# Performance work log

Measured on AMD Instinct MI355X. Metric: run time of the kernel, lower is better.

## Reference

```python
import jax, jax.numpy as jnp
import numpy as np


def _segmented_exclusive_cumsum(vals, seg_start_flags):
    """Exclusive cumsum of vals that resets at segment starts (flags True)."""
    def combine(a, b):
        va, fa = a
        vb, fb = b
        return (jnp.where(fb, vb, va + vb), fa | fb)
    inclusive, _ = jax.lax.associative_scan(combine, (vals, seg_start_flags))
    return inclusive - vals


def setup_inputs() -> dict:
    key = jax.random.key(0)
    k1, k2 = jax.random.split(key)
    n_rays = 65536
    samples_per_ray = 128  # average; ragged via sorted random ray ids
    n_pts = n_rays * samples_per_ray  # 8_388_608 sample points
    density = jax.random.normal(k1, (n_pts,), dtype=jnp.float32)
    ray_id = jnp.sort(jax.random.randint(k2, (n_pts,), 0, n_rays)).astype(jnp.int32)
    shift = jnp.float32(-3.0)      # self.act_shift
    interval = jnp.float32(0.5)    # stepsize * voxel_size_ratio
    return {"density": density, "shift": shift, "interval": interval,
            "ray_id": ray_id, "n_rays": n_rays}


def reference(density, shift, interval, ray_id, n_rays):
    # Raw2Alpha: alpha = 1 - exp(-softplus(density + shift) * interval)
    # log(1 - alpha) = -interval * softplus(density + shift)  (stable, no log of tiny)
    log_one_minus_alpha = -interval * jax.nn.softplus(density + shift)
    alpha = 1.0 - jnp.exp(log_one_minus_alpha)

    # Alphas2Weights: per-ray exclusive cumprod of (1 - alpha) in log space.
    # ray_id is sorted; segment starts where the ray id changes.
    seg_start = jnp.concatenate(
        [jnp.ones((1,), dtype=bool), ray_id[1:] != ray_id[:-1]])
    log_T = _segmented_exclusive_cumsum(log_one_minus_alpha, seg_start)
    T = jnp.exp(log_T)                      # transmittance before each sample
    weights = alpha * T                     # [n_pts]

    # alphainv_last[r] = prod over ray r of (1 - alpha) = residual transmittance
    log_total = jax.ops.segment_sum(log_one_minus_alpha, ray_id,
                                    num_segments=n_rays)
    alphainv_last = jnp.exp(log_total)      # [n_rays]; empty rays -> exp(0)=1
    return weights, alphainv_last
```

## Files before the change

kernel.cpp:

```cpp
#include <hip/hip_runtime.h>
#include <math.h>


#define LOG2E 1.4426950408889634f

typedef float vf4 __attribute__((ext_vector_type(4)));

__device__ __forceinline__ float exp2f_(float x) { return __builtin_amdgcn_exp2f(x); }
__device__ __forceinline__ float log2f_(float x) { return __builtin_amdgcn_logf(x); }
__device__ __forceinline__ float rsqf_(float x)  { return __builtin_amdgcn_rsqf(x); }

__device__ __forceinline__ float oma(float d, float sh2, float negc, bool fast) {
    const float y = fmaf(d, LOG2E, sh2);
    if (fast) return rsqf_(1.0f + exp2f_(y));
    const float sp = fmaxf(y, 0.f) + log2f_(1.f + exp2f_(-fabsf(y)));
    return exp2f_(negc * sp);
}

template <int CTRL, int RM>
__device__ __forceinline__ void seg_step(float& V, int& F) {
    const int vs_i = __builtin_amdgcn_update_dpp(
        0x3f800000, __builtin_bit_cast(int, V), CTRL, RM, 0xF, false);
    const int fs = __builtin_amdgcn_update_dpp(0, F, CTRL, RM, 0xF, false);
    const float vs = __builtin_bit_cast(float, vs_i);
    V = F ? V : vs * V;
    F = F | fs;
}

__device__ __forceinline__ float wave_prod_bcast(float x) {
#define STEPP(CTRL, RM)                                                        \
    { int t_ = __builtin_amdgcn_update_dpp(0x3f800000,                         \
          __builtin_bit_cast(int, x), CTRL, RM, 0xF, false);                   \
      x *= __builtin_bit_cast(float, t_); }
    STEPP(0x111, 0xF) STEPP(0x112, 0xF) STEPP(0x114, 0xF)
    STEPP(0x118, 0xF) STEPP(0x142, 0xA) STEPP(0x143, 0xC)
#undef STEPP
    return __builtin_bit_cast(float,
        __builtin_amdgcn_readlane(__builtin_bit_cast(int, x), 63));
}

__device__ __forceinline__ int wave_imax_bcast(int x) {
#define STEPM(CTRL, RM)                                                        \
    { int t_ = __builtin_amdgcn_update_dpp((int)0x80000000, x, CTRL, RM,       \
                                           0xF, false);                        \
      x = (x > t_) ? x : t_; }
    STEPM(0x111, 0xF) STEPM(0x112, 0xF) STEPM(0x114, 0xF)
    STEPM(0x118, 0xF) STEPM(0x142, 0xA) STEPM(0x143, 0xC)
#undef STEPM
    return __builtin_amdgcn_readlane(x, 63);
}

__global__ void __launch_bounds__(256)
fused_alpha_weights(const float* __restrict__ density,
                    const int*   __restrict__ ray_id,
                    const float* __restrict__ shift_p,
                    const float* __restrict__ interval_p,
                    float* __restrict__ weights,
                    float* __restrict__ alphainv,
                    int n_pts, int n_rays) {
    __shared__ int   s_first[256];
    __shared__ int   s_last[256];
    __shared__ float s_wv[4];
    __shared__ int   s_wf[4];
    __shared__ float s_red[4];
    __shared__ int   s_redi[4];

    const int t    = threadIdx.x;
    const int lane = t & 63;
    const int wid  = t >> 6;
    const int base = blockIdx.x << 10;
    const int idx0 = base + t * 4;

    const float shift = shift_p[0];
    const float c     = interval_p[0];
    const float sh2   = shift * LOG2E;
    const float negc  = -c;
    const bool  fast  = (c == 0.5f);

    int4 rid;  float4 den;
    bool v0, v1, v2, v3;
    if (idx0 + 4 <= n_pts) {
        rid = *reinterpret_cast<const int4*>(ray_id + idx0);
        den = *reinterpret_cast<const float4*>(density + idx0);
        v0 = v1 = v2 = v3 = true;
    } else {
        int r[4]; float d[4];
        #pragma unroll
        for (int k = 0; k < 4; ++k) {
            const int i = idx0 + k;
            const bool vv = (i < n_pts);
            r[k] = vv ? ray_id[i] : n_rays;
            d[k] = vv ? density[i] : 0.0f;
        }
        rid = make_int4(r[0], r[1], r[2], r[3]);
        den = make_float4(d[0], d[1], d[2], d[3]);
        v0 = (idx0 < n_pts); v1 = (idx0 + 1 < n_pts);
        v2 = (idx0 + 2 < n_pts); v3 = (idx0 + 3 < n_pts);
    }

    s_first[t] = rid.x;
    s_last[t]  = rid.w;
    __syncthreads();

    int next3;
    if (t < 255) next3 = s_first[t + 1];
    else         next3 = (base + 1024 < n_pts) ? ray_id[base + 1024] : n_rays;

    float carry0  = 1.0f;
    int   head_new = 1;
    if (base > 0) {
        const int rid_first = s_first[0];
        int lo = base, s0 = 0;
        for (;;) {
            const int wstart = lo - 256;
            const int i = wstart + t;
            const int v = (i >= 0) ? ray_id[i] : -1;
            const int cand = (v != rid_first) ? t : -1;
            const int wm = wave_imax_bcast(cand);
            if (lane == 0) s_redi[wid] = wm;
            __syncthreads();
            int m = s_redi[0];
            m = (s_redi[1] > m) ? s_redi[1] : m;
            m = (s_redi[2] > m) ? s_redi[2] : m;
            m = (s_redi[3] > m) ? s_redi[3] : m;
            __syncthreads();
            if (m >= 0) { s0 = wstart + m + 1; break; }
            lo = wstart;
        }
        head_new = (s0 == base) ? 1 : 0;
        for (int off = s0; off < base; off += 256) {
            const int i = off + t;
            const float aa = (i < base) ? oma(density[i], sh2, negc, fast) : 1.0f;
            const float wp = wave_prod_bcast(aa);
            if (lane == 0) s_red[wid] = wp;
            __syncthreads();
            carry0 *= s_red[0] * s_red[1] * s_red[2] * s_red[3];
            __syncthreads();
        }
    }

    float a0 = oma(den.x, sh2, negc, fast);
    float a1 = oma(den.y, sh2, negc, fast);
    float a2 = oma(den.z, sh2, negc, fast);
    float a3 = oma(den.w, sh2, negc, fast);
    a0 = v0 ? a0 : 1.0f;  a1 = v1 ? a1 : 1.0f;
    a2 = v2 ? a2 : 1.0f;  a3 = v3 ? a3 : 1.0f;

    const int prev_last = (t > 0) ? s_last[t - 1] : (head_new ? -1 : rid.x);
    const int f0 = (rid.x != prev_last);
    const int f1 = (rid.y != rid.x);
    const int f2 = (rid.z != rid.y);
    const int f3 = (rid.w != rid.z);

    float V = a0;  int F = f0;
    V = f1 ? a1 : V * a1;  F |= f1;
    V = f2 ? a2 : V * a2;  F |= f2;
    V = f3 ? a3 : V * a3;  F |= f3;

    float Vi = V;  int Fi = F;
    seg_step<0x111, 0xF>(Vi, Fi);
    seg_step<0x112, 0xF>(Vi, Fi);
    seg_step<0x114, 0xF>(Vi, Fi);
    seg_step<0x118, 0xF>(Vi, Fi);
    seg_step<0x142, 0xA>(Vi, Fi);
    seg_step<0x143, 0xC>(Vi, Fi);

    float Vx = __shfl_up(Vi, 1, 64);
    int   Fx = __shfl_up(Fi, 1, 64);
    if (lane == 0) { Vx = 1.0f; Fx = 0; }

    if (lane == 63) { s_wv[wid] = Vi; s_wf[wid] = Fi; }
    __syncthreads();
    float Ev = carry0;
    #pragma unroll
    for (int w2 = 0; w2 < 3; ++w2) {
        if (w2 < wid) {
            const float bv = s_wv[w2];  const int bf = s_wf[w2];
            Ev = bf ? bv : Ev * bv;
        }
    }
    Ev = Fx ? Vx : Ev * Vx;

    const float T0 = f0 ? 1.0f : Ev;
    const float T1 = f1 ? 1.0f : T0 * a0;
    const float T2 = f2 ? 1.0f : T1 * a1;
    const float T3 = f3 ? 1.0f : T2 * a2;
    const float e0 = T0 * a0, e1 = T1 * a1, e2 = T2 * a2, e3 = T3 * a3;

    if (idx0 + 4 <= n_pts) {
        vf4 w = { T0 - e0, T1 - e1, T2 - e2, T3 - e3 };
        __builtin_nontemporal_store(w, reinterpret_cast<vf4*>(weights + idx0));
    } else {
        if (v0) weights[idx0]     = T0 - e0;
        if (v1) weights[idx0 + 1] = T1 - e1;
        if (v2) weights[idx0 + 2] = T2 - e2;
        if (v3) weights[idx0 + 3] = T3 - e3;
    }

    if (v0 && rid.x != rid.y) {
        alphainv[rid.x] = e0;
        for (int q = rid.x + 1; q < rid.y; ++q) alphainv[q] = 1.0f;
    }
    if (v1 && rid.y != rid.z) {
        alphainv[rid.y] = e1;
        for (int q = rid.y + 1; q < rid.z; ++q) alphainv[q] = 1.0f;
    }
    if (v2 && rid.z != rid.w) {
        alphainv[rid.z] = e2;
        for (int q = rid.z + 1; q < rid.w; ++q) alphainv[q] = 1.0f;
    }
    if (v3 && rid.w != next3) {
        alphainv[rid.w] = e3;
        for (int q = rid.w + 1; q < next3; ++q) alphainv[q] = 1.0f;
    }
    if (idx0 == 0) {
        for (int q = 0; q < rid.x; ++q) alphainv[q] = 1.0f;
    }
}

extern "C" void kernel_launch(void* const* d_in, const int* in_sizes, int n_in,
                              void* d_out, int out_size, void* d_ws, size_t ws_size,
                              hipStream_t stream) {
    const float* density  = (const float*)d_in[0];
    const float* shift    = (const float*)d_in[1];
    const float* interval = (const float*)d_in[2];
    const int*   ray_id   = (const int*)d_in[3];
    const int n_pts  = in_sizes[0];
    const int n_rays = out_size - n_pts;

    float* weights  = (float*)d_out;
    float* alphainv = (float*)d_out + n_pts;

    const int grid = (n_pts + 1023) / 1024;
    fused_alpha_weights<<<grid, 256, 0, stream>>>(
        density, ray_id, shift, interval, weights, alphainv, n_pts, n_rays);
}
```

Measured before the change: 26.91 us.

## Prefetch block-carry window and neighbor ray ids to cut barriers and serial lookback

Drops the shared-memory staging of first/last ray ids; each thread now loads its neighbor ids directly from global memory. The preceding 256-element window (ids and densities) is loaded up front, alongside the tile's own loads, and its carry reduction is merged into the same barrier as the per-wave scan totals. The serial lookback loop only runs when the current ray started more than 256 samples before the block. This removes several __syncthreads and dependent global-load round trips from the critical path, at the cost of extra redundant global loads per thread.

```diff
diff --git a/kernel.cpp b/kernel.cpp
--- a/kernel.cpp
+++ b/kernel.cpp
@@ -58,8 +58,6 @@
                     float* __restrict__ weights,
                     float* __restrict__ alphainv,
                     int n_pts, int n_rays) {
-    __shared__ int   s_first[256];
-    __shared__ int   s_last[256];
     __shared__ float s_wv[4];
     __shared__ int   s_wf[4];
     __shared__ float s_red[4];
@@ -77,14 +75,15 @@
     const float negc  = -c;
     const bool  fast  = (c == 0.5f);
 
-    int4 rid;  float4 den;
+    int r[5]; float d[4];
     bool v0, v1, v2, v3;
     if (idx0 + 4 <= n_pts) {
-        rid = *reinterpret_cast<const int4*>(ray_id + idx0);
-        den = *reinterpret_cast<const float4*>(density + idx0);
+        const int4   ri = *reinterpret_cast<const int4*>(ray_id + idx0);
+        const float4 de = *reinterpret_cast<const float4*>(density + idx0);
+        r[0] = ri.x; r[1] = ri.y; r[2] = ri.z; r[3] = ri.w;
+        d[0] = de.x; d[1] = de.y; d[2] = de.z; d[3] = de.w;
         v0 = v1 = v2 = v3 = true;
     } else {
-        int r[4]; float d[4];
         #pragma unroll
         for (int k = 0; k < 4; ++k) {
             const int i = idx0 + k;
@@ -92,65 +91,32 @@
             r[k] = vv ? ray_id[i] : n_rays;
             d[k] = vv ? density[i] : 0.0f;
         }
-        rid = make_int4(r[0], r[1], r[2], r[3]);
-        den = make_float4(d[0], d[1], d[2], d[3]);
         v0 = (idx0 < n_pts); v1 = (idx0 + 1 < n_pts);
         v2 = (idx0 + 2 < n_pts); v3 = (idx0 + 3 < n_pts);
     }
-
-    s_first[t] = rid.x;
-    s_last[t]  = rid.w;
-    __syncthreads();
-
-    int next3;
-    if (t < 255) next3 = s_first[t + 1];
-    else         next3 = (base + 1024 < n_pts) ? ray_id[base + 1024] : n_rays;
-
-    float carry0  = 1.0f;
-    int   head_new = 1;
+    r[4] = (idx0 + 4 < n_pts) ? ray_id[idx0 + 4] : n_rays;
+    const int rprev = (idx0 == 0) ? -1
+                    : ((idx0 <= n_pts) ? ray_id[idx0 - 1] : n_rays);
+
+    int w_id = 0; float w_den = 0.0f; int rfirst = 0;
     if (base > 0) {
-        const int rid_first = s_first[0];
-        int lo = base, s0 = 0;
-        for (;;) {
-            const int wstart = lo - 256;
-            const int i = wstart + t;
-            const int v = (i >= 0) ? ray_id[i] : -1;
-            const int cand = (v != rid_first) ? t : -1;
-            const int wm = wave_imax_bcast(cand);
-            if (lane == 0) s_redi[wid] = wm;
-            __syncthreads();
-            int m = s_redi[0];
-            m = (s_redi[1] > m) ? s_redi[1] : m;
-            m = (s_redi[2] > m) ? s_redi[2] : m;
-            m = (s_redi[3] > m) ? s_redi[3] : m;
-            __syncthreads();
-            if (m >= 0) { s0 = wstart + m + 1; break; }
-            lo = wstart;
-        }
-        head_new = (s0 == base) ? 1 : 0;
-        for (int off = s0; off < base; off += 256) {
-            const int i = off + t;
-            const float aa = (i < base) ? oma(density[i], sh2, negc, fast) : 1.0f;
-            const float wp = wave_prod_bcast(aa);
-            if (lane == 0) s_red[wid] = wp;
-            __syncthreads();
-            carry0 *= s_red[0] * s_red[1] * s_red[2] * s_red[3];
-            __syncthreads();
-        }
-    }
-
-    float a0 = oma(den.x, sh2, negc, fast);
-    float a1 = oma(den.y, sh2, negc, fast);
-    float a2 = oma(den.z, sh2, negc, fast);
-    float a3 = oma(den.w, sh2, negc, fast);
+        const int wi = base - 256 + t;
+        w_id   = ray_id[wi];
+        w_den  = density[wi];
+        rfirst = ray_id[base];
+    }
+
+    float a0 = oma(d[0], sh2, negc, fast);
+    float a1 = oma(d[1], sh2, negc, fast);
+    float a2 = oma(d[2], sh2, negc, fast);
+    float a3 = oma(d[3], sh2, negc, fast);
     a0 = v0 ? a0 : 1.0f;  a1 = v1 ? a1 : 1.0f;
     a2 = v2 ? a2 : 1.0f;  a3 = v3 ? a3 : 1.0f;
 
-    const int prev_last = (t > 0) ? s_last[t - 1] : (head_new ? -1 : rid.x);
-    const int f0 = (rid.x != prev_last);
-    const int f1 = (rid.y != rid.x);
-    const int f2 = (rid.z != rid.y);
-    const int f3 = (rid.w != rid.z);
+    const int f0 = (r[0] != rprev);
+    const int f1 = (r[1] != r[0]);
+    const int f2 = (r[2] != r[1]);
+    const int f3 = (r[3] != r[2]);
 
     float V = a0;  int F = f0;
     V = f1 ? a1 : V * a1;  F |= f1;
@@ -165,12 +131,62 @@
     seg_step<0x142, 0xA>(Vi, Fi);
     seg_step<0x143, 0xC>(Vi, Fi);
 
+    if (lane == 63) { s_wv[wid] = Vi; s_wf[wid] = Fi; }
+    if (base > 0) {
+        const int cand = (w_id != rfirst) ? t : -1;
+        const int wm = wave_imax_bcast(cand);
+        if (lane == 0) s_redi[wid] = wm;
+    }
+    __syncthreads();
+
+    float carry0 = 1.0f;
+    if (base > 0) {
+        int m = s_redi[0];
+        m = (s_redi[1] > m) ? s_redi[1] : m;
+        m = (s_redi[2] > m) ? s_redi[2] : m;
+        m = (s_redi[3] > m) ? s_redi[3] : m;
+        float aa = oma(w_den, sh2, negc, fast);
+        if (m >= 0 && t <= m) aa = 1.0f;
+        const float wp = wave_prod_bcast(aa);
+        if (lane == 0) s_red[wid] = wp;
+        __syncthreads();
+        carry0 = s_red[0] * s_red[1] * s_red[2] * s_red[3];
+
+        if (m < 0) {
+            int lo = base - 256;
+            int s0 = -1;
+            while (s0 < 0) {
+                const int wstart = lo - 256;
+                const int i = wstart + t;
+                const int vv = (i >= 0) ? ray_id[i] : -1;
+                const int c2 = (vv != rfirst) ? t : -1;
+                const int wm2 = wave_imax_bcast(c2);
+                if (lane == 0) s_redi[wid] = wm2;
+                __syncthreads();
+                int m2 = s_redi[0];
+                m2 = (s_redi[1] > m2) ? s_redi[1] : m2;
+                m2 = (s_redi[2] > m2) ? s_redi[2] : m2;
+                m2 = (s_redi[3] > m2) ? s_redi[3] : m2;
+                __syncthreads();
+                if (m2 >= 0) s0 = wstart + m2 + 1; else lo = wstart;
+            }
+            for (int off = s0; off < base - 256; off += 256) {
+                const int i = off + t;
+                const float aa2 = (i < base - 256)
+                                ? oma(density[i], sh2, negc, fast) : 1.0f;
+                const float wp2 = wave_prod_bcast(aa2);
+                if (lane == 0) s_red[wid] = wp2;
+                __syncthreads();
+                carry0 *= s_red[0] * s_red[1] * s_red[2] * s_red[3];
+                __syncthreads();
+            }
+        }
+    }
+
     float Vx = __shfl_up(Vi, 1, 64);
     int   Fx = __shfl_up(Fi, 1, 64);
     if (lane == 0) { Vx = 1.0f; Fx = 0; }
 
-    if (lane == 63) { s_wv[wid] = Vi; s_wf[wid] = Fi; }
-    __syncthreads();
     float Ev = carry0;
     #pragma unroll
     for (int w2 = 0; w2 < 3; ++w2) {
@@ -182,10 +198,13 @@
     Ev = Fx ? Vx : Ev * Vx;
 
     const float T0 = f0 ? 1.0f : Ev;
-    const float T1 = f1 ? 1.0f : T0 * a0;
-    const float T2 = f2 ? 1.0f : T1 * a1;
-    const float T3 = f3 ? 1.0f : T2 * a2;
-    const float e0 = T0 * a0, e1 = T1 * a1, e2 = T2 * a2, e3 = T3 * a3;
+    const float e0 = T0 * a0;
+    const float T1 = f1 ? 1.0f : e0;
+    const float e1 = T1 * a1;
+    const float T2 = f2 ? 1.0f : e1;
+    const float e2 = T2 * a2;
+    const float T3 = f3 ? 1.0f : e2;
+    const float e3 = T3 * a3;
 
     if (idx0 + 4 <= n_pts) {
         vf4 w = { T0 - e0, T1 - e1, T2 - e2, T3 - e3 };
@@ -197,24 +216,24 @@
         if (v3) weights[idx0 + 3] = T3 - e3;
     }
 
-    if (v0 && rid.x != rid.y) {
-        alphainv[rid.x] = e0;
-        for (int q = rid.x + 1; q < rid.y; ++q) alphainv[q] = 1.0f;
-    }
-    if (v1 && rid.y != rid.z) {
-        alphainv[rid.y] = e1;
-        for (int q = rid.y + 1; q < rid.z; ++q) alphainv[q] = 1.0f;
-    }
-    if (v2 && rid.z != rid.w) {
-        alphainv[rid.z] = e2;
-        for (int q = rid.z + 1; q < rid.w; ++q) alphainv[q] = 1.0f;
-    }
-    if (v3 && rid.w != next3) {
-        alphainv[rid.w] = e3;
-        for (int q = rid.w + 1; q < next3; ++q) alphainv[q] = 1.0f;
+    if (v0 && r[0] != r[1]) {
+        alphainv[r[0]] = e0;
+        for (int q = r[0] + 1; q < r[1]; ++q) alphainv[q] = 1.0f;
+    }
+    if (v1 && r[1] != r[2]) {
+        alphainv[r[1]] = e1;
+        for (int q = r[1] + 1; q < r[2]; ++q) alphainv[q] = 1.0f;
+    }
+    if (v2 && r[2] != r[3]) {
+        alphainv[r[2]] = e2;
+        for (int q = r[2] + 1; q < r[3]; ++q) alphainv[q] = 1.0f;
+    }
+    if (v3 && r[3] != r[4]) {
+        alphainv[r[3]] = e3;
+        for (int q = r[3] + 1; q < r[4]; ++q) alphainv[q] = 1.0f;
     }
     if (idx0 == 0) {
-        for (int q = 0; q < rid.x; ++q) alphainv[q] = 1.0f;
+        for (int q = 0; q < r[0]; ++q) alphainv[q] = 1.0f;
     }
 }
 
```

New measurement: 24.47 us. 9.0% less time.
